# Optimization experiments

Hardware: AMD Instinct MI355X
Metric: run time of the kernel (lower is better)

## Reference

```python
import jax, jax.numpy as jnp
import numpy as np

_OFFS = np.array([(dx, dy, dz) for dx in (-1, 0, 1) for dy in (-1, 0, 1) for dz in (-1, 0, 1)], np.int64)


def setup_inputs() -> dict:
    rng = np.random.default_rng(0)
    B, G, NPTS = 2, 128, 100000
    # level-0 active voxel coords (batch, x, y, z)
    cs = []
    for b in range(B):
        xyz = np.unique(rng.integers(0, G, size=(NPTS, 3)), axis=0)
        cs.append(np.concatenate([np.full((len(xyz), 1), b, np.int64), xyz], 1))
    c0 = np.concatenate(cs, 0)
    c1 = np.unique(np.concatenate([c0[:, :1], c0[:, 1:] // 2], 1), axis=0)  # stride-2 coords
    c2 = np.unique(np.concatenate([c1[:, :1], c1[:, 1:] // 2], 1), axis=0)  # stride-4 coords

    def table(c, g):  # dense coordinate hash: coord -> row index, -1 if empty
        t = np.full((B, g, g, g), -1, np.int64)
        t[c[:, 0], c[:, 1], c[:, 2], c[:, 3]] = np.arange(len(c))
        return t

    t0, t1, t2 = table(c0, G), table(c1, G // 2), table(c2, G // 4)

    def kmap(out_c, tab, g, stride):  # kernel map for k=3 conv: [27, Nout], -1 = no neighbor
        base = out_c[:, 1:] * stride
        nbr = np.empty((27, len(out_c)), np.int32)
        for k, off in enumerate(_OFFS):
            p = base + off
            ok = ((p >= 0) & (p < g)).all(1)
            pc = np.clip(p, 0, g - 1)
            nbr[k] = np.where(ok, tab[out_c[:, 0], pc[:, 0], pc[:, 1], pc[:, 2]], -1)
        return nbr

    nbr0 = kmap(c0, t0, G, 1)        # enc1: submanifold, out coords == in coords
    nbr1 = kmap(c1, t0, G, 2)        # enc2: stride-2 downsample
    nbr2 = kmap(c2, t1, G // 2, 2)   # enc3: stride-2 downsample

    def upmap(fine_c, coarse_tab):   # k=2 s=2 transposed conv: unique parent + offset id
        q = fine_c[:, 1:] // 2
        idx = coarse_tab[fine_c[:, 0], q[:, 0], q[:, 1], q[:, 2]].astype(np.int32)
        r = fine_c[:, 1:] - 2 * q
        off = (r[:, 0] * 4 + r[:, 1] * 2 + r[:, 2]).astype(np.int32)
        return idx, off

    up1_idx, up1_off = upmap(c1, t2)  # dec2: level2 -> level1
    up0_idx, up0_off = upmap(c0, t1)  # dec1: level1 -> level0

    def w(shape):
        return jnp.asarray(rng.normal(0.0, 0.05, shape).astype(np.float32))

    feats = jnp.asarray(rng.normal(0.0, 1.0, (len(c0), 2)).astype(np.float32))
    return dict(
        feats=feats,
        W1=w((27, 2, 32)), W2=w((27, 32, 64)), W3=w((27, 64, 128)),
        W4=w((8, 128, 64)), W5=w((8, 64, 32)), Wout=w((32, 2)),
        g1=jnp.ones(32), b1=jnp.zeros(32), g2=jnp.ones(64), b2=jnp.zeros(64),
        g3=jnp.ones(128), b3=jnp.zeros(128), g4=jnp.ones(64), b4=jnp.zeros(64),
        g5=jnp.ones(32), b5=jnp.zeros(32),
        nbr0=jnp.asarray(nbr0), nbr1=jnp.asarray(nbr1), nbr2=jnp.asarray(nbr2),
        up1_idx=jnp.asarray(up1_idx), up1_off=jnp.asarray(up1_off),
        up0_idx=jnp.asarray(up0_idx), up0_off=jnp.asarray(up0_off),
    )


def _sconv(f, nbr, W):
    # implicit-GEMM sparse conv: gather per kernel offset, matmul, masked accumulate
    out = jnp.zeros((nbr.shape[1], W.shape[2]), f.dtype)
    for k in range(W.shape[0]):
        idx = nbr[k]
        g = jnp.where((idx >= 0)[:, None], f[jnp.maximum(idx, 0)], 0.0)
        out = out + g @ W[k]
    return out


def _upconv(f, pidx, poff, W):
    # k=2 s=2 transposed conv: each fine voxel has exactly one coarse parent + offset id in [0,8)
    g = f[pidx]
    out = jnp.zeros((g.shape[0], W.shape[2]), f.dtype)
    for k in range(8):
        out = out + jnp.where((poff == k)[:, None], g @ W[k], 0.0)
    return out


def _bn_relu(x, g, b):
    # training-mode BatchNorm over the voxel dim (biased var), then ReLU
    mu = x.mean(0)
    var = x.var(0)
    return jax.nn.relu((x - mu) * jax.lax.rsqrt(var + 1e-5) * g + b)


def reference(feats, W1, W2, W3, W4, W5, Wout, g1, b1, g2, b2, g3, b3, g4, b4, g5, b5,
              nbr0, nbr1, nbr2, up1_idx, up1_off, up0_idx, up0_off):
    e1 = _bn_relu(_sconv(feats, nbr0, W1), g1, b1)   # [N0, 32]
    e2 = _bn_relu(_sconv(e1, nbr1, W2), g2, b2)      # [N1, 64]
    e3 = _bn_relu(_sconv(e2, nbr2, W3), g3, b3)      # [N2, 128]
    d2 = _bn_relu(_upconv(e3, up1_idx, up1_off, W4), g4, b4)  # [N1, 64]
    d1 = _bn_relu(_upconv(d2, up0_idx, up0_off, W5), g5, b5)  # [N0, 32]
    return d1 @ Wout                                  # 1x1 conv, [N0, 2]
```

## Files before the change

kernel.cpp:

```cpp
#include <hip/hip_runtime.h>
#include <hip/hip_bf16.h>

typedef __attribute__((ext_vector_type(4))) float  f32x4;
typedef __attribute__((ext_vector_type(8))) short  short8;
typedef __attribute__((ext_vector_type(2))) float  flt2;
typedef long long ll;

__device__ __forceinline__ short f2bf(float f) {
    __hip_bfloat16 h = __float2bfloat16(f);
    short s; __builtin_memcpy(&s, &h, 2);
    return s;
}
__device__ __forceinline__ float bf2f(short s) {
    unsigned u = ((unsigned)(unsigned short)s) << 16;
    float f; __builtin_memcpy(&f, &u, 4);
    return f;
}
__device__ __forceinline__ void gload_lds16(const void* g, void* l) {
    __builtin_amdgcn_global_load_lds(
        (const __attribute__((address_space(1))) unsigned*)(g),
        (__attribute__((address_space(3))) unsigned*)(l),
        16, 0, 0);
}

__global__ void prep_kernel(const float* __restrict__ W1, const float* __restrict__ W2,
                            const float* __restrict__ W3, const float* __restrict__ W4,
                            const float* __restrict__ W5,
                            short* W1t, short* W2t, short* W3t, short* W4t, short* W5t) {
    int gid = blockIdx.x * 256 + threadIdx.x;
    if (gid < 32 * 64) {
        int co = gid >> 6, e = gid & 63;
        float v = 0.f;
        if (e < 54) { int k = e >> 1, ci = e & 1; v = W1[(k * 2 + ci) * 32 + co]; }
        W1t[gid] = f2bf(v);
        return;
    }
    int g = gid - 32 * 64;
    if (g < 28 * 2048) { int k = g / 2048, r = g % 2048, co = r >> 5, ci = r & 31;
        W2t[g] = (k < 27) ? f2bf(W2[((ll)k * 32 + ci) * 64 + co]) : (short)0; return; }
    g -= 28 * 2048;
    if (g < 28 * 8192) { int k = g / 8192, r = g % 8192, co = r >> 6, ci = r & 63;
        W3t[g] = (k < 27) ? f2bf(W3[((ll)k * 64 + ci) * 128 + co]) : (short)0; return; }
    g -= 28 * 8192;
    if (g < 8 * 64 * 128) { int k = g / (64*128), r = g % (64*128), co = r >> 7, ci = r & 127;
        W4t[g] = f2bf(W4[((ll)k * 128 + ci) * 64 + co]); return; }
    g -= 8 * 64 * 128;
    if (g < 8 * 32 * 64) { int k = g / (32*64), r = g % (32*64), co = r >> 6, ci = r & 63;
        W5t[g] = f2bf(W5[((ll)k * 64 + ci) * 32 + co]); return; }
}

__launch_bounds__(256)
__global__ void c1_kernel(const float* __restrict__ feats, const int* __restrict__ nbr,
                          const short* __restrict__ W1t, short* __restrict__ out,
                          float* __restrict__ part, int N) {
    __shared__ float sc[8 * 32];
    int tid = threadIdx.x, lane = tid & 63, wave = tid >> 6;
    int rb = blockIdx.x * 64 + wave * 16;
    int r = rb + (lane & 15);
    int rl = r < N ? r : N - 1;
    int seg = lane >> 4, l15 = lane & 15;
    f32x4 acc[2];
    acc[0] = (f32x4){0,0,0,0}; acc[1] = (f32x4){0,0,0,0};
    short8 a[2];
    #pragma unroll
    for (int kc = 0; kc < 2; ++kc) {
        #pragma unroll
        for (int j = 0; j < 4; ++j) {
            int k = kc * 16 + seg * 4 + j;
            flt2 f = (flt2){0.f, 0.f};
            if (k < 27) {
                int idx = nbr[(ll)k * N + rl];
                if (idx >= 0) f = *(const flt2*)(feats + 2 * (ll)idx);
            }
            a[kc][2*j]   = f2bf(f[0]);
            a[kc][2*j+1] = f2bf(f[1]);
        }
    }
    #pragma unroll
    for (int kc = 0; kc < 2; ++kc)
        #pragma unroll
        for (int c = 0; c < 2; ++c) {
            short8 b = *(const short8*)(W1t + (c*16 + l15) * 64 + kc * 32 + seg * 8);
            acc[c] = __builtin_amdgcn_mfma_f32_16x16x32_bf16(a[kc], b, acc[c], 0, 0, 0);
        }
    int r0 = rb + seg * 4;
    #pragma unroll
    for (int c = 0; c < 2; ++c) {
        int col = c * 16 + l15;
        #pragma unroll
        for (int j = 0; j < 4; ++j)
            if (r0 + j < N) out[(ll)(r0 + j) * 32 + col] = f2bf(acc[c][j]);
    }
    float s[2], q[2];
    #pragma unroll
    for (int c = 0; c < 2; ++c) { s[c] = 0.f; q[c] = 0.f; }
    #pragma unroll
    for (int c = 0; c < 2; ++c)
        #pragma unroll
        for (int j = 0; j < 4; ++j) {
            float v = (r0 + j < N) ? acc[c][j] : 0.f;
            s[c] += v; q[c] += v * v;
        }
    #pragma unroll
    for (int c = 0; c < 2; ++c) {
        s[c] += __shfl_xor(s[c], 16); q[c] += __shfl_xor(q[c], 16);
        s[c] += __shfl_xor(s[c], 32); q[c] += __shfl_xor(q[c], 32);
    }
    if (lane < 16) {
        #pragma unroll
        for (int c = 0; c < 2; ++c) {
            sc[(wave * 2 + 0) * 32 + c * 16 + l15] = s[c];
            sc[(wave * 2 + 1) * 32 + c * 16 + l15] = q[c];
        }
    }
    __syncthreads();
    for (int i = tid; i < 32; i += 256) {
        float ss = sc[0*32+i] + sc[2*32+i] + sc[4*32+i] + sc[6*32+i];
        float qq = sc[1*32+i] + sc[3*32+i] + sc[5*32+i] + sc[7*32+i];
        part[(ll)blockIdx.x * 64 + i]      = ss;
        part[(ll)blockIdx.x * 64 + 32 + i] = qq;
    }
}

template<int CIN, int COLS, int RG, int MINW>
__launch_bounds__(256, MINW)
__global__ void msconv5_kernel(const short* __restrict__ inb, const int* __restrict__ nbr,
                               const short* __restrict__ Wt, short* __restrict__ out,
                               float* __restrict__ part, int N, int zoff) {
    constexpr int KC = CIN / 32, NT = COLS / 16;
    constexpr int CPK = COLS * CIN / 8, BIT = CPK / 256;
    constexpr int WST = COLS * CIN;
    constexpr int SH = (CIN == 32) ? 6 : 7;
    constexpr int P = RG + BIT + RG * KC;
    __shared__ __align__(16) short lb[3][WST];

    const int tid = threadIdx.x, lane = tid & 63, wave = tid >> 6;
    const int seg = lane >> 4, l15 = lane & 15;
    const int wrb = blockIdx.x * (64 * RG) + wave * (16 * RG);
    const char* inB = (const char*)inb;

    int rl[RG];
    #pragma unroll
    for (int rg = 0; rg < RG; ++rg) {
        int r = wrb + rg * 16 + l15;
        rl[rg] = r < N ? r : N - 1;
    }

    auto rawIdx = [&](int k, int (&ix)[RG]) {
        #pragma unroll
        for (int rg = 0; rg < RG; ++rg) ix[rg] = nbr[(ll)k * N + rl[rg]];
    };
    auto mkoff = [&](const int (&ix)[RG], int (&o)[RG]) {
        #pragma unroll
        for (int rg = 0; rg < RG; ++rg) o[rg] = (ix[rg] >= 0) ? (ix[rg] << SH) : zoff;
    };
    auto stage = [&](int kn, int buf) {
        #pragma unroll
        for (int it = 0; it < BIT; ++it) {
            int q = it * 256 + tid;
            int co = q % COLS, sg = (q / COLS) & 3, kc = q / (COLS * 4);
            gload_lds16(Wt + (ll)kn * WST + co * CIN + kc * 32 + sg * 8, &lb[buf][q * 8]);
        }
    };
    auto ldA = [&](short8 (&a)[RG][KC], const int (&o)[RG]) {
        #pragma unroll
        for (int rg = 0; rg < RG; ++rg) {
            const char* base = inB + o[rg];
            #pragma unroll
            for (int kc = 0; kc < KC; ++kc)
                a[rg][kc] = *(const short8*)(base + kc * 64 + seg * 16);
        }
    };

    f32x4 acc[RG][NT];
    #pragma unroll
    for (int rg = 0; rg < RG; ++rg)
        #pragma unroll
        for (int c = 0; c < NT; ++c) acc[rg][c] = (f32x4){0.f, 0.f, 0.f, 0.f};

    auto compute = [&](int buf, short8 (&a)[RG][KC]) {
        #pragma unroll
        for (int kc = 0; kc < KC; ++kc)
            #pragma unroll
            for (int c = 0; c < NT; ++c) {
                short8 b = *(const short8*)&lb[buf][((kc * 4 + seg) * COLS + c * 16 + l15) * 8];
                #pragma unroll
                for (int rg = 0; rg < RG; ++rg)
                    acc[rg][c] = __builtin_amdgcn_mfma_f32_16x16x32_bf16(
                        a[rg][kc], b, acc[rg][c], 0, 0, 0);
            }
    };

    short8 aA[RG][KC], aB[RG][KC];
    int iF[RG], offC[RG];

    {
        int i0[RG], i1[RG], o0[RG];
        rawIdx(0, i0); rawIdx(1, i1); rawIdx(2, iF);
        mkoff(i0, o0); mkoff(i1, offC);
        stage(0, 0); stage(1, 1);
        __builtin_amdgcn_sched_barrier(0);
        ldA(aA, o0);
        __builtin_amdgcn_sched_barrier(0);
        asm volatile("s_waitcnt vmcnt(%0) lgkmcnt(0)" :: "n"(BIT + RG * KC) : "memory");
        __builtin_amdgcn_s_barrier();
        __builtin_amdgcn_sched_barrier(0);
    }

    #pragma unroll
    for (int k = 0; k < 27; ++k) {
        int iN[RG];
        {
            int kq = (k + 3 < 27) ? (k + 3) : 26;
            rawIdx(kq, iN);
            int kt = (k + 2 < 27) ? (k + 2) : 27;
            stage(kt, (k + 2) % 3);
        }
        __builtin_amdgcn_sched_barrier(0);
        if (k & 1) ldA(aA, offC); else ldA(aB, offC);
        __builtin_amdgcn_sched_barrier(0);
        if (k & 1) compute(k % 3, aB); else compute(k % 3, aA);
        __builtin_amdgcn_sched_barrier(0);
        asm volatile("s_waitcnt vmcnt(%0) lgkmcnt(0)" :: "n"(P) : "memory");
        __builtin_amdgcn_s_barrier();
        __builtin_amdgcn_sched_barrier(0);
        mkoff(iF, offC);
        #pragma unroll
        for (int rg = 0; rg < RG; ++rg) iF[rg] = iN[rg];
    }

    #pragma unroll
    for (int rg = 0; rg < RG; ++rg)
        #pragma unroll
        for (int c = 0; c < NT; ++c) {
            int col = c * 16 + l15;
            #pragma unroll
            for (int j = 0; j < 4; ++j) {
                int rr = wrb + rg * 16 + seg * 4 + j;
                if (rr < N) out[(ll)rr * COLS + col] = f2bf(acc[rg][c][j]);
            }
        }

    float s[NT], q[NT];
    #pragma unroll
    for (int c = 0; c < NT; ++c) { s[c] = 0.f; q[c] = 0.f; }
    #pragma unroll
    for (int rg = 0; rg < RG; ++rg)
        #pragma unroll
        for (int c = 0; c < NT; ++c)
            #pragma unroll
            for (int j = 0; j < 4; ++j) {
                int rr = wrb + rg * 16 + seg * 4 + j;
                float v = (rr < N) ? acc[rg][c][j] : 0.f;
                s[c] += v; q[c] += v * v;
            }
    #pragma unroll
    for (int c = 0; c < NT; ++c) {
        s[c] += __shfl_xor(s[c], 16); q[c] += __shfl_xor(q[c], 16);
        s[c] += __shfl_xor(s[c], 32); q[c] += __shfl_xor(q[c], 32);
    }
    float* sc = (float*)&lb[0][0];
    if (lane < 16) {
        #pragma unroll
        for (int c = 0; c < NT; ++c) {
            sc[(wave * 2 + 0) * COLS + c * 16 + l15] = s[c];
            sc[(wave * 2 + 1) * COLS + c * 16 + l15] = q[c];
        }
    }
    __syncthreads();
    for (int i = tid; i < COLS; i += 256) {
        float ss = sc[0*COLS+i] + sc[2*COLS+i] + sc[4*COLS+i] + sc[6*COLS+i];
        float qq = sc[1*COLS+i] + sc[3*COLS+i] + sc[5*COLS+i] + sc[7*COLS+i];
        part[(ll)blockIdx.x * 2 * COLS + i]        = ss;
        part[(ll)blockIdx.x * 2 * COLS + COLS + i] = qq;
    }
}

__global__ void dcount_kernel(const int* __restrict__ poff, int* __restrict__ cnt, int N) {
    __shared__ int lc[8];
    if (threadIdx.x < 8) lc[threadIdx.x] = 0;
    __syncthreads();
    int r = blockIdx.x * 256 + threadIdx.x;
    if (r < N) atomicAdd(&lc[poff[r]], 1);
    __syncthreads();
    if (threadIdx.x < 8 && lc[threadIdx.x]) atomicAdd(&cnt[threadIdx.x], lc[threadIdx.x]);
}

__global__ void dprefix_kernel(const int* __restrict__ cnt, int* __restrict__ bases,
                               int* __restrict__ kofb, int* __restrict__ perm, int nblk) {
    __shared__ int base[9];
    if (threadIdx.x == 0) {
        int b = 0;
        for (int k = 0; k < 8; ++k) { base[k] = b; b += (cnt[k] + 63) & ~63; }
        base[8] = b;
        for (int k = 0; k < 9; ++k) bases[k] = base[k];
    }
    __syncthreads();
    int nb = base[8] >> 6;
    for (int i = threadIdx.x; i < nblk; i += 256) {
        int k = -1;
        if (i < nb) {
            int rb = i << 6; k = 0;
            while (rb >= base[k + 1]) ++k;
        }
        kofb[i] = k;
    }
    for (int k = 0; k < 8; ++k) {
        int s = base[k] + cnt[k], e = base[k + 1];
        for (int i = s + threadIdx.x; i < e; i += 256) perm[i] = -1;
    }
}

__global__ void dscatter_kernel(const int* __restrict__ poff, const int* __restrict__ bases,
                                int* __restrict__ cur, int* __restrict__ perm, int N) {
    __shared__ int lc[8], lbs[8];
    if (threadIdx.x < 8) lc[threadIdx.x] = 0;
    __syncthreads();
    int r = blockIdx.x * 256 + threadIdx.x;
    int k = 0, myl = 0;
    if (r < N) { k = poff[r]; myl = atomicAdd(&lc[k], 1); }
    __syncthreads();
    if (threadIdx.x < 8) lbs[threadIdx.x] = atomicAdd(&cur[threadIdx.x], lc[threadIdx.x]);
    __syncthreads();
    if (r < N) perm[bases[k] + lbs[k] + myl] = r;
}

template<int CIN, int COUT>
__launch_bounds__(256)
__global__ void gdec_kernel(const short* __restrict__ inb, const int* __restrict__ perm,
                            const int* __restrict__ kofb, const int* __restrict__ pidx,
                            const short* __restrict__ Wt, const short* __restrict__ zrow,
                            short* __restrict__ out, float* __restrict__ part) {
    constexpr int KC = CIN / 32, NT = COUT / 16;
    constexpr int CPK = COUT * CIN / 8, BIT = CPK / 256;
    __shared__ __align__(16) short lb[COUT * CIN];
    const int tid = threadIdx.x, lane = tid & 63, wave = tid >> 6;
    int k = kofb[blockIdx.x];
    if (k < 0) {
        for (int i = tid; i < 2 * COUT; i += 256) part[(ll)blockIdx.x * 2 * COUT + i] = 0.f;
        return;
    }
    const int seg = lane >> 4, l15 = lane & 15;
    const int wrb = blockIdx.x * 64 + wave * 16;
    int rl = wrb + l15;
    int pr = perm[rl];
    int idx = pr < 0 ? -1 : pidx[pr];

    #pragma unroll
    for (int it = 0; it < BIT; ++it) {
        int q = it * 256 + tid;
        int co = q % COUT, sg = (q / COUT) & 3, kc = q / (COUT * 4);
        gload_lds16(Wt + ((ll)k * COUT + co) * CIN + kc * 32 + sg * 8, &lb[q * 8]);
    }
    short8 a[KC];
    const short* base = (idx < 0) ? zrow : (inb + (ll)idx * CIN);
    #pragma unroll
    for (int kc = 0; kc < KC; ++kc)
        a[kc] = *(const short8*)(base + kc * 32 + seg * 8);

    f32x4 acc[NT];
    #pragma unroll
    for (int c = 0; c < NT; ++c) acc[c] = (f32x4){0.f, 0.f, 0.f, 0.f};
    __syncthreads();
    #pragma unroll
    for (int kc = 0; kc < KC; ++kc)
        #pragma unroll
        for (int c = 0; c < NT; ++c) {
            short8 b = *(const short8*)&lb[((kc * 4 + seg) * COUT + c * 16 + l15) * 8];
            acc[c] = __builtin_amdgcn_mfma_f32_16x16x32_bf16(a[kc], b, acc[c], 0, 0, 0);
        }
    #pragma unroll
    for (int j = 0; j < 4; ++j) {
        int prs = __shfl(pr, seg * 4 + j, 64);
        if (prs >= 0) {
            #pragma unroll
            for (int c = 0; c < NT; ++c)
                out[(ll)prs * COUT + c * 16 + l15] = f2bf(acc[c][j]);
        }
    }
    float s[NT], q[NT];
    #pragma unroll
    for (int c = 0; c < NT; ++c) { s[c] = 0.f; q[c] = 0.f; }
    #pragma unroll
    for (int c = 0; c < NT; ++c)
        #pragma unroll
        for (int j = 0; j < 4; ++j) { float v = acc[c][j]; s[c] += v; q[c] += v * v; }
    #pragma unroll
    for (int c = 0; c < NT; ++c) {
        s[c] += __shfl_xor(s[c], 16); q[c] += __shfl_xor(q[c], 16);
        s[c] += __shfl_xor(s[c], 32); q[c] += __shfl_xor(q[c], 32);
    }
    __syncthreads();
    float* sc = (float*)lb;
    if (lane < 16) {
        #pragma unroll
        for (int c = 0; c < NT; ++c) {
            sc[(wave * 2 + 0) * COUT + c * 16 + l15] = s[c];
            sc[(wave * 2 + 1) * COUT + c * 16 + l15] = q[c];
        }
    }
    __syncthreads();
    for (int i = tid; i < COUT; i += 256) {
        float ss = sc[0*COUT+i] + sc[2*COUT+i] + sc[4*COUT+i] + sc[6*COUT+i];
        float qq = sc[1*COUT+i] + sc[3*COUT+i] + sc[5*COUT+i] + sc[7*COUT+i];
        part[(ll)blockIdx.x * 2 * COUT + i]        = ss;
        part[(ll)blockIdx.x * 2 * COUT + COUT + i] = qq;
    }
}

__global__ void red2_kernel(const float* __restrict__ part, int nblk,
                            const float* __restrict__ g, const float* __restrict__ bb,
                            float* __restrict__ A, float* __restrict__ B, int C, int N) {
    int c = blockIdx.x;
    float s = 0.f, q = 0.f;
    for (int i = threadIdx.x; i < nblk; i += 256) {
        s += part[(ll)i * 2 * C + c];
        q += part[(ll)i * 2 * C + C + c];
    }
    __shared__ float ls[256], lq[256];
    ls[threadIdx.x] = s; lq[threadIdx.x] = q;
    __syncthreads();
    for (int str = 128; str >= 1; str >>= 1) {
        if (threadIdx.x < str) {
            ls[threadIdx.x] += ls[threadIdx.x + str];
            lq[threadIdx.x] += lq[threadIdx.x + str];
        }
        __syncthreads();
    }
    if (threadIdx.x == 0) {
        float inv = 1.0f / (float)N;
        float mu = ls[0] * inv, var = lq[0] * inv - mu * mu;
        float a = g[c] * rsqrtf(var + 1e-5f);
        A[c] = a; B[c] = bb[c] - mu * a;
    }
}

template<int C>
__global__ void bnrelu_kernel(const short* __restrict__ x, const float* __restrict__ A,
                              const float* __restrict__ B, short* __restrict__ out, int N) {
    constexpr int CPR = C / 8;
    int i = blockIdx.x * 256 + threadIdx.x;
    if (i >= N * CPR) return;
    int r = i / CPR, ch = i - r * CPR;
    short8 v = *(const short8*)(x + (ll)r * C + ch * 8);
    short8 o;
    #pragma unroll
    for (int j = 0; j < 8; ++j) {
        int c = ch * 8 + j;
        float y = fmaf(bf2f(v[j]), A[c], B[c]);
        o[j] = f2bf(y > 0.f ? y : 0.f);
    }
    *(short8*)(out + (ll)r * C + ch * 8) = o;
}

__global__ void outk_kernel(const short* __restrict__ z, const float* __restrict__ A,
                            const float* __restrict__ B, const float* __restrict__ Wout,
                            float* __restrict__ out, int N) {
    __shared__ float w[64], sa[32], sb[32];
    if (threadIdx.x < 64) w[threadIdx.x] = Wout[threadIdx.x];
    if (threadIdx.x < 32) { sa[threadIdx.x] = A[threadIdx.x]; sb[threadIdx.x] = B[threadIdx.x]; }
    __syncthreads();
    int r = blockIdx.x * 256 + threadIdx.x;
    if (r >= N) return;
    const short* zp = z + (ll)r * 32;
    float o0 = 0.f, o1 = 0.f;
    #pragma unroll
    for (int s4 = 0; s4 < 4; ++s4) {
        short8 v = *(const short8*)(zp + s4 * 8);
        #pragma unroll
        for (int j = 0; j < 8; ++j) {
            int c = s4 * 8 + j;
            float y = fmaf(bf2f(v[j]), sa[c], sb[c]);
            y = y > 0.f ? y : 0.f;
            o0 = fmaf(y, w[2*c], o0);
            o1 = fmaf(y, w[2*c+1], o1);
        }
    }
    out[(ll)r * 2]     = o0;
    out[(ll)r * 2 + 1] = o1;
}

extern "C" void kernel_launch(void* const* d_in, const int* in_sizes, int n_in,
                              void* d_out, int out_size, void* d_ws, size_t ws_size,
                              hipStream_t stream) {
    const float* feats = (const float*)d_in[0];
    const float* W1 = (const float*)d_in[1];
    const float* W2 = (const float*)d_in[2];
    const float* W3 = (const float*)d_in[3];
    const float* W4 = (const float*)d_in[4];
    const float* W5 = (const float*)d_in[5];
    const float* Wout = (const float*)d_in[6];
    const float* g1 = (const float*)d_in[7],  *b1 = (const float*)d_in[8];
    const float* g2 = (const float*)d_in[9],  *b2 = (const float*)d_in[10];
    const float* g3 = (const float*)d_in[11], *b3 = (const float*)d_in[12];
    const float* g4 = (const float*)d_in[13], *b4 = (const float*)d_in[14];
    const float* g5 = (const float*)d_in[15], *b5 = (const float*)d_in[16];
    const int* nbr0 = (const int*)d_in[17];
    const int* nbr1 = (const int*)d_in[18];
    const int* nbr2 = (const int*)d_in[19];
    const int* up1_idx = (const int*)d_in[20];
    const int* up1_off = (const int*)d_in[21];
    const int* up0_idx = (const int*)d_in[22];
    const int* up0_off = (const int*)d_in[23];

    const int N0 = in_sizes[0] / 2;
    const int N1 = in_sizes[20];
    const int N2 = in_sizes[19] / 27;

    char* cur = (char*)d_ws;
    auto alloc = [&](size_t bytes) { char* p = cur; cur += (bytes + 255) & ~255ULL; return p; };
    auto cdiv = [](ll a, ll b) { return (int)((a + b - 1) / b); };

    float* stats = (float*)alloc(4096);
    float* A1 = stats,       *B1c = stats + 32;
    float* A2 = stats + 64,  *B2c = stats + 128;
    float* A3 = stats + 192, *B3c = stats + 320;
    float* A4 = stats + 448, *B4c = stats + 512;
    float* A5 = stats + 576, *B5c = stats + 608;
    short* zrow  = (short*)((char*)stats + 2560);
    int*   cnt4  = (int*)((char*)stats + 3072);
    int*   cur4  = (int*)((char*)stats + 3104);
    int*   cnt5  = (int*)((char*)stats + 3136);
    int*   cur5  = (int*)((char*)stats + 3168);
    int*   bas4  = (int*)((char*)stats + 3200);
    int*   bas5  = (int*)((char*)stats + 3264);

    float* part = (float*)alloc(2 * 1024 * 1024);

    size_t zmax = (size_t)N1 * 64;
    if ((size_t)N0 * 32  > zmax) zmax = (size_t)N0 * 32;
    if ((size_t)N2 * 128 > zmax) zmax = (size_t)N2 * 128;
    short* zb  = (short*)alloc(zmax * 2);
    short* e1b = (short*)alloc((size_t)N0 * 32 * 2);
    short* e2b = (short*)alloc((size_t)N1 * 64 * 2);
    short* e3b = (short*)alloc((size_t)N2 * 128 * 2);
    short* d2b = (short*)alloc((size_t)N1 * 64 * 2);
    short* W1t = (short*)alloc(32 * 64 * 2);
    short* W2t = (short*)alloc((size_t)28 * 64 * 32 * 2);
    short* W3t = (short*)alloc((size_t)28 * 128 * 64 * 2);
    short* W4t = (short*)alloc((size_t)8 * 64 * 128 * 2);
    short* W5t = (short*)alloc((size_t)8 * 32 * 64 * 2);

    const int gridL4 = cdiv((ll)N1 + 512, 64);
    const int gridL5 = cdiv((ll)N0 + 512, 64);
    int* perm4 = (int*)alloc((size_t)gridL4 * 64 * 4);
    int* kofb4 = (int*)alloc((size_t)gridL4 * 4);
    int* perm5 = (int*)alloc((size_t)gridL5 * 64 * 4);
    int* kofb5 = (int*)alloc((size_t)gridL5 * 4);

    const int zoff1 = (int)((ll)((char*)zrow - (char*)e1b));
    const int zoff2 = (int)((ll)((char*)zrow - (char*)e2b));

    const int nblk1 = cdiv(N0, 64);
    const int nblk2 = cdiv(N1, 128);
    const int nblk3 = cdiv(N2, 128);

    hipMemsetAsync((char*)stats + 2560, 0, 640, stream);

    prep_kernel<<<cdiv(2048 + 28*2048 + 28*8192 + 65536 + 16384, 256), 256, 0, stream>>>(
        W1, W2, W3, W4, W5, W1t, W2t, W3t, W4t, W5t);

    dcount_kernel<<<cdiv(N1, 256), 256, 0, stream>>>(up1_off, cnt4, N1);
    dprefix_kernel<<<1, 256, 0, stream>>>(cnt4, bas4, kofb4, perm4, gridL4);
    dscatter_kernel<<<cdiv(N1, 256), 256, 0, stream>>>(up1_off, bas4, cur4, perm4, N1);
    dcount_kernel<<<cdiv(N0, 256), 256, 0, stream>>>(up0_off, cnt5, N0);
    dprefix_kernel<<<1, 256, 0, stream>>>(cnt5, bas5, kofb5, perm5, gridL5);
    dscatter_kernel<<<cdiv(N0, 256), 256, 0, stream>>>(up0_off, bas5, cur5, perm5, N0);

    c1_kernel<<<nblk1, 256, 0, stream>>>(feats, nbr0, W1t, zb, part, N0);
    red2_kernel<<<32, 256, 0, stream>>>(part, nblk1, g1, b1, A1, B1c, 32, N0);
    bnrelu_kernel<32><<<cdiv((ll)N0 * 4, 256), 256, 0, stream>>>(zb, A1, B1c, e1b, N0);

    msconv5_kernel<32, 64, 2, 4><<<nblk2, 256, 0, stream>>>(e1b, nbr1, W2t, zb, part, N1, zoff1);
    red2_kernel<<<64, 256, 0, stream>>>(part, nblk2, g2, b2, A2, B2c, 64, N1);
    bnrelu_kernel<64><<<cdiv((ll)N1 * 8, 256), 256, 0, stream>>>(zb, A2, B2c, e2b, N1);

    msconv5_kernel<64, 128, 2, 3><<<nblk3, 256, 0, stream>>>(e2b, nbr2, W3t, zb, part, N2, zoff2);
    red2_kernel<<<128, 256, 0, stream>>>(part, nblk3, g3, b3, A3, B3c, 128, N2);
    bnrelu_kernel<128><<<cdiv((ll)N2 * 16, 256), 256, 0, stream>>>(zb, A3, B3c, e3b, N2);

    gdec_kernel<128, 64><<<gridL4, 256, 0, stream>>>(e3b, perm4, kofb4, up1_idx, W4t, zrow, zb, part);
    red2_kernel<<<64, 256, 0, stream>>>(part, gridL4, g4, b4, A4, B4c, 64, N1);
    bnrelu_kernel<64><<<cdiv((ll)N1 * 8, 256), 256, 0, stream>>>(zb, A4, B4c, d2b, N1);

    gdec_kernel<64, 32><<<gridL5, 256, 0, stream>>>(d2b, perm5, kofb5, up0_idx, W5t, zrow, zb, part);
    red2_kernel<<<32, 256, 0, stream>>>(part, gridL5, g5, b5, A5, B5c, 32, N0);
    outk_kernel<<<cdiv(N0, 256), 256, 0, stream>>>(zb, A5, B5c, Wout, (float*)d_out, N0);
}
```

Measured before the change: 259.8 us.

## Double-buffer sparse conv weights, XCD-swizzle block ids, batch decoder prep kernels

The sparse conv kernel moves from a triple-buffered LDS weight pipeline with a prefetch distance of two to a double-buffered one with a prefetch distance of one. This cuts LDS use, which may allow more resident blocks, but leaves less time to hide each stage's load. All conv and decoder kernels now remap block ids with an XCD swizzle so neighbouring row tiles land on the same XCD, aiming for better L2 locality. The count, prefix and scatter kernels for the two decoder levels are each merged into one launch, removing three launches.

```diff
diff --git a/kernel.cpp b/kernel.cpp
--- a/kernel.cpp
+++ b/kernel.cpp
@@ -21,6 +21,11 @@
         (const __attribute__((address_space(1))) unsigned*)(g),
         (__attribute__((address_space(3))) unsigned*)(l),
         16, 0, 0);
+}
+__device__ __forceinline__ int xcd_swz(int bid, int nwg) {
+    int q8 = nwg >> 3, r8 = nwg & 7;
+    int xcd = bid & 7, j = bid >> 3;
+    return (xcd < r8 ? xcd * (q8 + 1) : r8 * (q8 + 1) + (xcd - r8) * q8) + j;
 }
 
 __global__ void prep_kernel(const float* __restrict__ W1, const float* __restrict__ W2,
@@ -54,8 +59,9 @@
                           const short* __restrict__ W1t, short* __restrict__ out,
                           float* __restrict__ part, int N) {
     __shared__ float sc[8 * 32];
+    const int wgid = xcd_swz(blockIdx.x, gridDim.x);
     int tid = threadIdx.x, lane = tid & 63, wave = tid >> 6;
-    int rb = blockIdx.x * 64 + wave * 16;
+    int rb = wgid * 64 + wave * 16;
     int r = rb + (lane & 15);
     int rl = r < N ? r : N - 1;
     int seg = lane >> 4, l15 = lane & 15;
@@ -117,26 +123,26 @@
     for (int i = tid; i < 32; i += 256) {
         float ss = sc[0*32+i] + sc[2*32+i] + sc[4*32+i] + sc[6*32+i];
         float qq = sc[1*32+i] + sc[3*32+i] + sc[5*32+i] + sc[7*32+i];
-        part[(ll)blockIdx.x * 64 + i]      = ss;
-        part[(ll)blockIdx.x * 64 + 32 + i] = qq;
+        part[(ll)wgid * 64 + i]      = ss;
+        part[(ll)wgid * 64 + 32 + i] = qq;
     }
 }
 
 template<int CIN, int COLS, int RG, int MINW>
 __launch_bounds__(256, MINW)
-__global__ void msconv5_kernel(const short* __restrict__ inb, const int* __restrict__ nbr,
+__global__ void msconv7_kernel(const short* __restrict__ inb, const int* __restrict__ nbr,
                                const short* __restrict__ Wt, short* __restrict__ out,
                                float* __restrict__ part, int N, int zoff) {
     constexpr int KC = CIN / 32, NT = COLS / 16;
     constexpr int CPK = COLS * CIN / 8, BIT = CPK / 256;
     constexpr int WST = COLS * CIN;
     constexpr int SH = (CIN == 32) ? 6 : 7;
-    constexpr int P = RG + BIT + RG * KC;
-    __shared__ __align__(16) short lb[3][WST];
-
+    __shared__ __align__(16) short lb[2][WST];
+
+    const int wgid = xcd_swz(blockIdx.x, gridDim.x);
     const int tid = threadIdx.x, lane = tid & 63, wave = tid >> 6;
     const int seg = lane >> 4, l15 = lane & 15;
-    const int wrb = blockIdx.x * (64 * RG) + wave * (16 * RG);
+    const int wrb = wgid * (64 * RG) + wave * (16 * RG);
     const char* inB = (const char*)inb;
 
     int rl[RG];
@@ -198,11 +204,11 @@
         int i0[RG], i1[RG], o0[RG];
         rawIdx(0, i0); rawIdx(1, i1); rawIdx(2, iF);
         mkoff(i0, o0); mkoff(i1, offC);
-        stage(0, 0); stage(1, 1);
+        stage(0, 0);
         __builtin_amdgcn_sched_barrier(0);
         ldA(aA, o0);
         __builtin_amdgcn_sched_barrier(0);
-        asm volatile("s_waitcnt vmcnt(%0) lgkmcnt(0)" :: "n"(BIT + RG * KC) : "memory");
+        asm volatile("s_waitcnt vmcnt(%0) lgkmcnt(0)" :: "n"(RG * KC) : "memory");
         __builtin_amdgcn_s_barrier();
         __builtin_amdgcn_sched_barrier(0);
     }
@@ -210,23 +216,26 @@
     #pragma unroll
     for (int k = 0; k < 27; ++k) {
         int iN[RG];
-        {
-            int kq = (k + 3 < 27) ? (k + 3) : 26;
-            rawIdx(kq, iN);
-            int kt = (k + 2 < 27) ? (k + 2) : 27;
-            stage(kt, (k + 2) % 3);
-        }
-        __builtin_amdgcn_sched_barrier(0);
-        if (k & 1) ldA(aA, offC); else ldA(aB, offC);
-        __builtin_amdgcn_sched_barrier(0);
-        if (k & 1) compute(k % 3, aB); else compute(k % 3, aA);
-        __builtin_amdgcn_sched_barrier(0);
-        asm volatile("s_waitcnt vmcnt(%0) lgkmcnt(0)" :: "n"(P) : "memory");
-        __builtin_amdgcn_s_barrier();
-        __builtin_amdgcn_sched_barrier(0);
-        mkoff(iF, offC);
-        #pragma unroll
-        for (int rg = 0; rg < RG; ++rg) iF[rg] = iN[rg];
+        if (k + 1 < 27) {
+            if (k + 3 < 27) rawIdx(k + 3, iN);
+            __builtin_amdgcn_sched_barrier(0);
+            stage(k + 1, (k + 1) & 1);
+            __builtin_amdgcn_sched_barrier(0);
+            if (k & 1) ldA(aA, offC); else ldA(aB, offC);
+            __builtin_amdgcn_sched_barrier(0);
+        }
+        if (k & 1) compute(1, aB); else compute(0, aA);
+        if (k + 1 < 27) {
+            __builtin_amdgcn_sched_barrier(0);
+            asm volatile("s_waitcnt vmcnt(%0) lgkmcnt(0)" :: "n"(RG * KC) : "memory");
+            __builtin_amdgcn_s_barrier();
+            __builtin_amdgcn_sched_barrier(0);
+            mkoff(iF, offC);
+            if (k + 3 < 27) {
+                #pragma unroll
+                for (int rg = 0; rg < RG; ++rg) iF[rg] = iN[rg];
+            }
+        }
     }
 
     #pragma unroll
@@ -259,6 +268,7 @@
         s[c] += __shfl_xor(s[c], 16); q[c] += __shfl_xor(q[c], 16);
         s[c] += __shfl_xor(s[c], 32); q[c] += __shfl_xor(q[c], 32);
     }
+    __syncthreads();
     float* sc = (float*)&lb[0][0];
     if (lane < 16) {
         #pragma unroll
@@ -271,12 +281,16 @@
     for (int i = tid; i < COLS; i += 256) {
         float ss = sc[0*COLS+i] + sc[2*COLS+i] + sc[4*COLS+i] + sc[6*COLS+i];
         float qq = sc[1*COLS+i] + sc[3*COLS+i] + sc[5*COLS+i] + sc[7*COLS+i];
-        part[(ll)blockIdx.x * 2 * COLS + i]        = ss;
-        part[(ll)blockIdx.x * 2 * COLS + COLS + i] = qq;
-    }
-}
-
-__global__ void dcount_kernel(const int* __restrict__ poff, int* __restrict__ cnt, int N) {
+        part[(ll)wgid * 2 * COLS + i]        = ss;
+        part[(ll)wgid * 2 * COLS + COLS + i] = qq;
+    }
+}
+
+__global__ void dcountB_kernel(const int* __restrict__ poffA, int NA, int* __restrict__ cntA,
+                               const int* __restrict__ poffB, int NB, int* __restrict__ cntB) {
+    const int* poff = blockIdx.y ? poffB : poffA;
+    int* cnt = blockIdx.y ? cntB : cntA;
+    int N = blockIdx.y ? NB : NA;
     __shared__ int lc[8];
     if (threadIdx.x < 8) lc[threadIdx.x] = 0;
     __syncthreads();
@@ -286,8 +300,15 @@
     if (threadIdx.x < 8 && lc[threadIdx.x]) atomicAdd(&cnt[threadIdx.x], lc[threadIdx.x]);
 }
 
-__global__ void dprefix_kernel(const int* __restrict__ cnt, int* __restrict__ bases,
-                               int* __restrict__ kofb, int* __restrict__ perm, int nblk) {
+__global__ void dprefixB_kernel(const int* __restrict__ cntA, int* basesA, int* kofbA,
+                                int* permA, int nblkA,
+                                const int* __restrict__ cntB, int* basesB, int* kofbB,
+                                int* permB, int nblkB) {
+    const int* cnt = blockIdx.x ? cntB : cntA;
+    int* bases = blockIdx.x ? basesB : basesA;
+    int* kofb  = blockIdx.x ? kofbB  : kofbA;
+    int* perm  = blockIdx.x ? permB  : permA;
+    int nblk   = blockIdx.x ? nblkB  : nblkA;
     __shared__ int base[9];
     if (threadIdx.x == 0) {
         int b = 0;
@@ -311,8 +332,15 @@
     }
 }
 
-__global__ void dscatter_kernel(const int* __restrict__ poff, const int* __restrict__ bases,
-                                int* __restrict__ cur, int* __restrict__ perm, int N) {
+__global__ void dscatterB_kernel(const int* __restrict__ poffA, const int* basesA,
+                                 int* curA, int* permA, int NA,
+                                 const int* __restrict__ poffB, const int* basesB,
+                                 int* curB, int* permB, int NB) {
+    const int* poff = blockIdx.y ? poffB : poffA;
+    const int* bases = blockIdx.y ? basesB : basesA;
+    int* curp = blockIdx.y ? curB : curA;
+    int* perm = blockIdx.y ? permB : permA;
+    int N = blockIdx.y ? NB : NA;
     __shared__ int lc[8], lbs[8];
     if (threadIdx.x < 8) lc[threadIdx.x] = 0;
     __syncthreads();
@@ -320,7 +348,7 @@
     int k = 0, myl = 0;
     if (r < N) { k = poff[r]; myl = atomicAdd(&lc[k], 1); }
     __syncthreads();
-    if (threadIdx.x < 8) lbs[threadIdx.x] = atomicAdd(&cur[threadIdx.x], lc[threadIdx.x]);
+    if (threadIdx.x < 8) lbs[threadIdx.x] = atomicAdd(&curp[threadIdx.x], lc[threadIdx.x]);
     __syncthreads();
     if (r < N) perm[bases[k] + lbs[k] + myl] = r;
 }
@@ -334,14 +362,15 @@
     constexpr int KC = CIN / 32, NT = COUT / 16;
     constexpr int CPK = COUT * CIN / 8, BIT = CPK / 256;
     __shared__ __align__(16) short lb[COUT * CIN];
+    const int wgid = xcd_swz(blockIdx.x, gridDim.x);
     const int tid = threadIdx.x, lane = tid & 63, wave = tid >> 6;
-    int k = kofb[blockIdx.x];
+    int k = kofb[wgid];
     if (k < 0) {
-        for (int i = tid; i < 2 * COUT; i += 256) part[(ll)blockIdx.x * 2 * COUT + i] = 0.f;
+        for (int i = tid; i < 2 * COUT; i += 256) part[(ll)wgid * 2 * COUT + i] = 0.f;
         return;
     }
     const int seg = lane >> 4, l15 = lane & 15;
-    const int wrb = blockIdx.x * 64 + wave * 16;
+    const int wrb = wgid * 64 + wave * 16;
     int rl = wrb + l15;
     int pr = perm[rl];
     int idx = pr < 0 ? -1 : pidx[pr];
@@ -403,8 +432,8 @@
     for (int i = tid; i < COUT; i += 256) {
         float ss = sc[0*COUT+i] + sc[2*COUT+i] + sc[4*COUT+i] + sc[6*COUT+i];
         float qq = sc[1*COUT+i] + sc[3*COUT+i] + sc[5*COUT+i] + sc[7*COUT+i];
-        part[(ll)blockIdx.x * 2 * COUT + i]        = ss;
-        part[(ll)blockIdx.x * 2 * COUT + COUT + i] = qq;
+        part[(ll)wgid * 2 * COUT + i]        = ss;
+        part[(ll)wgid * 2 * COUT + COUT + i] = qq;
     }
 }
 
@@ -560,22 +589,24 @@
     prep_kernel<<<cdiv(2048 + 28*2048 + 28*8192 + 65536 + 16384, 256), 256, 0, stream>>>(
         W1, W2, W3, W4, W5, W1t, W2t, W3t, W4t, W5t);
 
-    dcount_kernel<<<cdiv(N1, 256), 256, 0, stream>>>(up1_off, cnt4, N1);
-    dprefix_kernel<<<1, 256, 0, stream>>>(cnt4, bas4, kofb4, perm4, gridL4);
-    dscatter_kernel<<<cdiv(N1, 256), 256, 0, stream>>>(up1_off, bas4, cur4, perm4, N1);
-    dcount_kernel<<<cdiv(N0, 256), 256, 0, stream>>>(up0_off, cnt5, N0);
-    dprefix_kernel<<<1, 256, 0, stream>>>(cnt5, bas5, kofb5, perm5, gridL5);
-    dscatter_kernel<<<cdiv(N0, 256), 256, 0, stream>>>(up0_off, bas5, cur5, perm5, N0);
+    {
+        int gx = cdiv(N1 > N0 ? N1 : N0, 256);
+        dcountB_kernel<<<dim3(gx, 2), 256, 0, stream>>>(up1_off, N1, cnt4, up0_off, N0, cnt5);
+        dprefixB_kernel<<<2, 256, 0, stream>>>(cnt4, bas4, kofb4, perm4, gridL4,
+                                               cnt5, bas5, kofb5, perm5, gridL5);
+        dscatterB_kernel<<<dim3(gx, 2), 256, 0, stream>>>(up1_off, bas4, cur4, perm4, N1,
+                                                          up0_off, bas5, cur5, perm5, N0);
+    }
 
     c1_kernel<<<nblk1, 256, 0, stream>>>(feats, nbr0, W1t, zb, part, N0);
     red2_kernel<<<32, 256, 0, stream>>>(part, nblk1, g1, b1, A1, B1c, 32, N0);
     bnrelu_kernel<32><<<cdiv((ll)N0 * 4, 256), 256, 0, stream>>>(zb, A1, B1c, e1b, N0);
 
-    msconv5_kernel<32, 64, 2, 4><<<nblk2, 256, 0, stream>>>(e1b, nbr1, W2t, zb, part, N1, zoff1);
+    msconv7_kernel<32, 64, 2, 4><<<nblk2, 256, 0, stream>>>(e1b, nbr1, W2t, zb, part, N1, zoff1);
     red2_kernel<<<64, 256, 0, stream>>>(part, nblk2, g2, b2, A2, B2c, 64, N1);
     bnrelu_kernel<64><<<cdiv((ll)N1 * 8, 256), 256, 0, stream>>>(zb, A2, B2c, e2b, N1);
 
-    msconv5_kernel<64, 128, 2, 3><<<nblk3, 256, 0, stream>>>(e2b, nbr2, W3t, zb, part, N2, zoff2);
+    msconv7_kernel<64, 128, 2, 3><<<nblk3, 256, 0, stream>>>(e2b, nbr2, W3t, zb, part, N2, zoff2);
     red2_kernel<<<128, 256, 0, stream>>>(part, nblk3, g3, b3, A3, B3c, 128, N2);
     bnrelu_kernel<128><<<cdiv((ll)N2 * 16, 256), 256, 0, stream>>>(zb, A3, B3c, e3b, N2);
 
```

Measured after the change: 240.8 us. 7.3% less time.
